# Kernel optimization log

Hardware: AMD Instinct MI355X
Metric: run time of the kernel (lower is better)

## Reference

```python
import jax, jax.numpy as jnp
import numpy as np

N, V = 256, 128000
TEMPERATURE = 1.0
TOP_P = 0.9


def setup_inputs() -> dict:
    key = jax.random.key(0)
    k1, k2 = jax.random.split(key)
    logits = jax.random.normal(k1, (N, V), dtype=jnp.float32) * 4.0
    u = jax.random.uniform(k2, (N, V), dtype=jnp.float32, minval=1e-9, maxval=1.0)
    gumbel = -jnp.log(-jnp.log(u))  # Gumbel(0,1) noise for categorical sampling
    return {"logits": logits, "gumbel": gumbel, "top_k": 50}


def reference(logits, gumbel, top_k):
    fmin = jnp.finfo(logits.dtype).min
    # sanitize non-finite logits (matches torch.where(isfinite, ...))
    logits = jnp.where(jnp.isfinite(logits), logits, fmin)
    # temperature > 0 path
    logits = logits / TEMPERATURE
    # ---- top-p (nucleus) filtering ----
    sort_idx = jnp.argsort(-logits, axis=-1)                     # descending order indices [N,V]
    sorted_logits = jnp.take_along_axis(logits, sort_idx, axis=-1)
    cum_probs = jnp.cumsum(jax.nn.softmax(sorted_logits, axis=-1), axis=-1)
    remove_sorted = cum_probs > TOP_P
    # shift right by one; always keep the top-1 token
    remove_sorted = jnp.concatenate(
        [jnp.zeros_like(remove_sorted[..., :1]), remove_sorted[..., :-1]], axis=-1)
    # scatter mask back to original order via inverse permutation
    inv_perm = jnp.argsort(sort_idx, axis=-1)
    mask = jnp.take_along_axis(remove_sorted, inv_perm, axis=-1)
    logits = jnp.where(mask, fmin, logits)
    # ---- top-k filtering ----
    kth = jax.lax.top_k(logits, top_k)[0][..., -1:]              # k-th largest per row
    logits = jnp.where(logits < kth, fmin, logits)
    # ---- softmax + categorical sample (Gumbel-max trick) ----
    probs = jax.nn.softmax(logits, axis=-1)
    x0 = jnp.argmax(logits + gumbel, axis=-1)                    # ~ Categorical(probs)
    initial_confidence = jnp.take_along_axis(probs, x0[..., None], axis=-1)[..., 0]
    confidence = initial_confidence
    return confidence, x0.astype(jnp.int32), initial_confidence
```

## Files before the change

kernel.cpp:

```cpp
#include <hip/hip_runtime.h>
#include <cstdint>
#include <cfloat>
#include <math.h>

#define VCAB 128000
#define NROWS 256
#define NTH 1024
#define NBUCK 8192
#define CAP2 2560
#define CKN 1024

__device__ __forceinline__ unsigned mono(float f) {
    unsigned u = __float_as_uint(f);
    return (u & 0x80000000u) ? ~u : (u | 0x80000000u);
}
__device__ __forceinline__ float unmono(unsigned k) {
    return __uint_as_float((k & 0x80000000u) ? (k ^ 0x80000000u) : ~k);
}

__device__ __forceinline__ unsigned find_bstar_wave(const unsigned* hist, int startb, int lane) {
    int hb = startb;
    unsigned cum = 0u;
    for (int it = 0; it < 200; ++it) {
        int b = hb - lane;
        unsigned c = (b >= 0 && b < NBUCK) ? hist[b] : 0u;
        unsigned p = c;
        #pragma unroll
        for (int off = 1; off < 64; off <<= 1) {
            unsigned q = __shfl_up(p, off, 64);
            if (lane >= off) p += q;
        }
        unsigned long long mm = __ballot(cum + p >= 64u);
        if (mm) {
            int l = __builtin_ctzll(mm);
            int b2 = hb - l;
            return (unsigned)(b2 > 0 ? b2 : 0);
        }
        cum += __shfl(p, 63, 64);
        hb -= 64;
        if (hb < 0) return 0u;
    }
    return 0u;
}

__global__ __launch_bounds__(NTH) void sampler_kernel(
    const float* __restrict__ logits,
    const float* __restrict__ gumbel,
    const int* __restrict__ topk_p,
    float* __restrict__ out)
{
    const int row = blockIdx.x;
    const int t = threadIdx.x;
    const size_t base = (size_t)row * VCAB;
    const float4* rowv = reinterpret_cast<const float4*>(logits + base);

    __shared__ unsigned hist[NBUCK];
    __shared__ unsigned long long cand[CAP2];
    __shared__ unsigned long long ck[CKN];
    __shared__ unsigned candCnt, candCnt2;
    __shared__ unsigned sh_bsamp, sh_bfin;
    __shared__ float red[16], red2[16];
    __shared__ float sh_msamp, sh_m0, sh_S;

    #pragma unroll
    for (int j = 0; j < NBUCK / NTH; ++j) hist[t + j * NTH] = 0u;
    if (t == 0) { candCnt = 0u; candCnt2 = 0u; }
    __syncthreads();

    float smax = -FLT_MAX;
    #pragma unroll
    for (int ii = 0; ii < 2; ++ii) {
        float4 x = rowv[t + ii * NTH];
        float vs[4] = {x.x, x.y, x.z, x.w};
        #pragma unroll
        for (int c = 0; c < 4; ++c) {
            float v = vs[c];
            if (!(fabsf(v) <= FLT_MAX)) v = -FLT_MAX;
            smax = fmaxf(smax, v);
            atomicAdd(&hist[mono(v) >> 19], 1u);
        }
    }
    for (int off = 32; off > 0; off >>= 1) smax = fmaxf(smax, __shfl_xor(smax, off, 64));
    if ((t & 63) == 0) red[t >> 6] = smax;
    __syncthreads();
    if (t < 16) {
        float m = red[t];
        #pragma unroll
        for (int off = 8; off > 0; off >>= 1) m = fmaxf(m, __shfl_xor(m, off, 16));
        if (t == 0) sh_msamp = m;
    }
    __syncthreads();
    const float msamp = sh_msamp;

    if (t < 64) {
        unsigned b = find_bstar_wave(hist, (int)(mono(msamp) >> 19), t);
        if (t == 0) sh_bsamp = b;
    }
    __syncthreads();
    const float thrV = unmono(sh_bsamp << 19);
    #pragma unroll
    for (int j = 0; j < NBUCK / NTH; ++j) hist[t + j * NTH] = 0u;
    __syncthreads();

    float sacc[4] = {0.f, 0.f, 0.f, 0.f};
    float lacc[4] = {-FLT_MAX, -FLT_MAX, -FLT_MAX, -FLT_MAX};
    for (int i = t; i < VCAB / 4; i += NTH) {
        float4 x = rowv[i];
        float vs[4] = {x.x, x.y, x.z, x.w};
        #pragma unroll
        for (int c = 0; c < 4; ++c) {
            float v = vs[c];
            if (!(fabsf(v) <= FLT_MAX)) v = -FLT_MAX;
            lacc[c] = fmaxf(lacc[c], v);
            sacc[c] += __expf(v - msamp);
            if (v >= thrV) {
                unsigned k = mono(v);
                atomicAdd(&hist[k >> 19], 1u);
                unsigned pos = atomicAdd(&candCnt, 1u);
                if (pos < CAP2)
                    cand[pos] = ((unsigned long long)k << 32) |
                                (unsigned long long)(~(unsigned)(i * 4 + c));
            }
        }
    }
    float s = (sacc[0] + sacc[1]) + (sacc[2] + sacc[3]);
    float lmax = fmaxf(fmaxf(lacc[0], lacc[1]), fmaxf(lacc[2], lacc[3]));
    for (int off = 32; off > 0; off >>= 1) {
        lmax = fmaxf(lmax, __shfl_xor(lmax, off, 64));
        s += __shfl_xor(s, off, 64);
    }
    if ((t & 63) == 0) { red[t >> 6] = lmax; red2[t >> 6] = s; }
    __syncthreads();
    if (t < 16) {
        float m = red[t], z = red2[t];
        #pragma unroll
        for (int off = 8; off > 0; off >>= 1) {
            m = fmaxf(m, __shfl_xor(m, off, 16));
            z += __shfl_xor(z, off, 16);
        }
        if (t == 0) { sh_m0 = m; sh_S = z; }
    }
    __syncthreads();
    const float S = sh_S;

    if (t < 64) {
        unsigned b = find_bstar_wave(hist, (int)(mono(sh_m0) >> 19), t);
        if (t == 0) sh_bfin = b;
    }
    __syncthreads();
    const unsigned bfin = sh_bfin;

    ck[t] = 0ull;
    __syncthreads();
    if (candCnt <= CAP2) {
        const unsigned nc = candCnt;
        for (unsigned j = t; j < nc; j += NTH) {
            unsigned long long e = cand[j];
            if ((unsigned)(e >> 51) >= bfin) {
                unsigned pos = atomicAdd(&candCnt2, 1u);
                if (pos < CKN) ck[pos] = e;
            }
        }
    } else {
        const float thr2 = unmono(bfin << 19);
        for (int i = t; i < VCAB / 4; i += NTH) {
            float4 x = rowv[i];
            float vs[4] = {x.x, x.y, x.z, x.w};
            #pragma unroll
            for (int c = 0; c < 4; ++c) {
                float v = vs[c];
                if (!(fabsf(v) <= FLT_MAX)) v = -FLT_MAX;
                if (v >= thr2) {
                    unsigned pos = atomicAdd(&candCnt2, 1u);
                    if (pos < CKN)
                        ck[pos] = ((unsigned long long)mono(v) << 32) |
                                  (unsigned long long)(~(unsigned)(i * 4 + c));
                }
            }
        }
    }
    __syncthreads();

    const unsigned nc2 = candCnt2 < (unsigned)CKN ? candCnt2 : (unsigned)CKN;
    const int nsort = (nc2 <= 256u) ? 256 : CKN;
    for (int k = 2; k <= nsort; k <<= 1) {
        for (int j = k >> 1; j > 0; j >>= 1) {
            __syncthreads();
            if (t < nsort) {
                int l = t ^ j;
                if (l > t) {
                    unsigned long long a = ck[t], b = ck[l];
                    bool up = ((t & k) == 0);
                    if (up ? (a < b) : (a > b)) { ck[t] = b; ck[l] = a; }
                }
            }
        }
    }
    __syncthreads();

    if (t < 64) {
        unsigned long long key = ck[t];
        float v = unmono((unsigned)(key >> 32));
        int idx = (int)(~(unsigned)key);
        int K = *topk_p;
        K = min(max(K, 1), 64);

        float p = expf(v - msamp) / S;
        float pref = p;
        for (int off = 1; off < 64; off <<= 1) {
            float xx = __shfl_up(pref, off, 64);
            if (t >= off) pref += xx;
        }
        float Eex = pref - p;
        int M = (int)__popcll(__ballot(Eex <= 0.9f));

        int Mfinal;
        if (M >= K) {
            float kth = __shfl(v, K - 1, 64);
            int J = (int)__popcll(__ballot(v >= kth));
            Mfinal = min(M, J);
        } else {
            Mfinal = M;
        }

        bool act = (t < Mfinal);
        float g  = act ? gumbel[base + (size_t)idx] : 0.f;
        float tt = act ? (v + g) : -FLT_MAX;
        int   ti = act ? idx : 0x7FFFFFFF;
        float bv = v;
        float bt = tt; int bi = ti;
        for (int off = 32; off > 0; off >>= 1) {
            float ot = __shfl_xor(bt, off, 64);
            int   oi = __shfl_xor(bi, off, 64);
            float ov = __shfl_xor(bv, off, 64);
            if (ot > bt || (ot == bt && oi < bi)) { bt = ot; bi = oi; bv = ov; }
        }
        float e = act ? expf(v - msamp) : 0.f;
        float Z = e;
        for (int off = 32; off > 0; off >>= 1) Z += __shfl_xor(Z, off, 64);

        if (t == 0) {
            float conf = expf(bv - msamp) / Z;
            out[row] = conf;
            out[NROWS + row] = (float)bi;
            out[2 * NROWS + row] = conf;
        }
    }
}

extern "C" void kernel_launch(void* const* d_in, const int* in_sizes, int n_in,
                              void* d_out, int out_size, void* d_ws, size_t ws_size,
                              hipStream_t stream) {
    const float* logits = (const float*)d_in[0];
    const float* gumbel = (const float*)d_in[1];
    const int*   topk   = (const int*)d_in[2];
    float* out = (float*)d_out;
    sampler_kernel<<<NROWS, NTH, 0, stream>>>(logits, gumbel, topk, out);
}
```

Baseline: 252.5 us.

## Use per-wave ballot-compacted candidate buffers and build histogram from candidates

```diff
diff --git a/kernel.cpp b/kernel.cpp
--- a/kernel.cpp
+++ b/kernel.cpp
@@ -6,8 +6,9 @@
 #define VCAB 128000
 #define NROWS 256
 #define NTH 1024
-#define NBUCK 8192
-#define CAP2 2560
+#define NWAVE 16
+#define NBUCK 4096
+#define CAPW 256
 #define CKN 1024
 
 __device__ __forceinline__ unsigned mono(float f) {
@@ -21,7 +22,7 @@
 __device__ __forceinline__ unsigned find_bstar_wave(const unsigned* hist, int startb, int lane) {
     int hb = startb;
     unsigned cum = 0u;
-    for (int it = 0; it < 200; ++it) {
+    for (int it = 0; it < 80; ++it) {
         int b = hb - lane;
         unsigned c = (b >= 0 && b < NBUCK) ? hist[b] : 0u;
         unsigned p = c;
@@ -51,20 +52,22 @@
 {
     const int row = blockIdx.x;
     const int t = threadIdx.x;
+    const int lane = t & 63;
+    const int wid = t >> 6;
     const size_t base = (size_t)row * VCAB;
     const float4* rowv = reinterpret_cast<const float4*>(logits + base);
 
     __shared__ unsigned hist[NBUCK];
-    __shared__ unsigned long long cand[CAP2];
+    __shared__ unsigned long long candW[NWAVE * CAPW];
     __shared__ unsigned long long ck[CKN];
-    __shared__ unsigned candCnt, candCnt2;
+    __shared__ unsigned wcnts[NWAVE];
+    __shared__ unsigned candCnt2;
     __shared__ unsigned sh_bsamp, sh_bfin;
     __shared__ float red[16], red2[16];
     __shared__ float sh_msamp, sh_m0, sh_S;
 
     #pragma unroll
     for (int j = 0; j < NBUCK / NTH; ++j) hist[t + j * NTH] = 0u;
-    if (t == 0) { candCnt = 0u; candCnt2 = 0u; }
     __syncthreads();
 
     float smax = -FLT_MAX;
@@ -77,11 +80,11 @@
             float v = vs[c];
             if (!(fabsf(v) <= FLT_MAX)) v = -FLT_MAX;
             smax = fmaxf(smax, v);
-            atomicAdd(&hist[mono(v) >> 19], 1u);
+            atomicAdd(&hist[mono(v) >> 20], 1u);
         }
     }
     for (int off = 32; off > 0; off >>= 1) smax = fmaxf(smax, __shfl_xor(smax, off, 64));
-    if ((t & 63) == 0) red[t >> 6] = smax;
+    if (lane == 0) red[wid] = smax;
     __syncthreads();
     if (t < 16) {
         float m = red[t];
@@ -93,43 +96,67 @@
     const float msamp = sh_msamp;
 
     if (t < 64) {
-        unsigned b = find_bstar_wave(hist, (int)(mono(msamp) >> 19), t);
+        unsigned b = find_bstar_wave(hist, (int)(mono(msamp) >> 20), lane);
         if (t == 0) sh_bsamp = b;
     }
     __syncthreads();
-    const float thrV = unmono(sh_bsamp << 19);
+    const float thrV = unmono(sh_bsamp << 20);
     #pragma unroll
     for (int j = 0; j < NBUCK / NTH; ++j) hist[t + j * NTH] = 0u;
     __syncthreads();
 
     float sacc[4] = {0.f, 0.f, 0.f, 0.f};
     float lacc[4] = {-FLT_MAX, -FLT_MAX, -FLT_MAX, -FLT_MAX};
-    for (int i = t; i < VCAB / 4; i += NTH) {
-        float4 x = rowv[i];
-        float vs[4] = {x.x, x.y, x.z, x.w};
-        #pragma unroll
-        for (int c = 0; c < 4; ++c) {
-            float v = vs[c];
-            if (!(fabsf(v) <= FLT_MAX)) v = -FLT_MAX;
-            lacc[c] = fmaxf(lacc[c], v);
-            sacc[c] += __expf(v - msamp);
-            if (v >= thrV) {
-                unsigned k = mono(v);
-                atomicAdd(&hist[k >> 19], 1u);
-                unsigned pos = atomicAdd(&candCnt, 1u);
-                if (pos < CAP2)
-                    cand[pos] = ((unsigned long long)k << 32) |
-                                (unsigned long long)(~(unsigned)(i * 4 + c));
-            }
-        }
-    }
+    unsigned wcnt = 0u;
+
+#define PROC(XV, IDX)                                                          \
+    {                                                                          \
+        float vs[4] = {(XV).x, (XV).y, (XV).z, (XV).w};                        \
+        _Pragma("unroll")                                                      \
+        for (int c = 0; c < 4; ++c) {                                          \
+            float v = vs[c];                                                   \
+            if (!(fabsf(v) <= FLT_MAX)) v = -FLT_MAX;                          \
+            lacc[c] = fmaxf(lacc[c], v);                                       \
+            sacc[c] += __expf(v - msamp);                                      \
+            bool p = (v >= thrV);                                              \
+            unsigned long long mb = __ballot(p);                               \
+            if (mb) {                                                          \
+                if (p) {                                                       \
+                    unsigned prefix = __builtin_amdgcn_mbcnt_hi(               \
+                        (unsigned)(mb >> 32),                                  \
+                        __builtin_amdgcn_mbcnt_lo((unsigned)mb, 0u));          \
+                    unsigned pos = wcnt + prefix;                              \
+                    if (pos < CAPW)                                            \
+                        candW[wid * CAPW + pos] =                              \
+                            ((unsigned long long)mono(v) << 32) |              \
+                            (unsigned long long)(~(unsigned)((IDX) * 4 + c));  \
+                }                                                              \
+                wcnt += (unsigned)__popcll(mb);                                \
+            }                                                                  \
+        }                                                                      \
+    }
+
+    int i = t;
+    for (; i + NTH < VCAB / 4; i += 2 * NTH) {
+        float4 xa = rowv[i];
+        float4 xb = rowv[i + NTH];
+        PROC(xa, i);
+        PROC(xb, i + NTH);
+    }
+    for (; i < VCAB / 4; i += NTH) {
+        float4 xa = rowv[i];
+        PROC(xa, i);
+    }
+#undef PROC
+
+    if (lane == 0) wcnts[wid] = wcnt;
     float s = (sacc[0] + sacc[1]) + (sacc[2] + sacc[3]);
     float lmax = fmaxf(fmaxf(lacc[0], lacc[1]), fmaxf(lacc[2], lacc[3]));
     for (int off = 32; off > 0; off >>= 1) {
         lmax = fmaxf(lmax, __shfl_xor(lmax, off, 64));
         s += __shfl_xor(s, off, 64);
     }
-    if ((t & 63) == 0) { red[t >> 6] = lmax; red2[t >> 6] = s; }
+    if (lane == 0) { red[wid] = lmax; red2[wid] = s; }
     __syncthreads();
     if (t < 16) {
         float m = red[t], z = red2[t];
@@ -143,28 +170,56 @@
     __syncthreads();
     const float S = sh_S;
 
+    bool ovf = false;
+    #pragma unroll
+    for (int w = 0; w < NWAVE; ++w) ovf |= (wcnts[w] > (unsigned)CAPW);
+
+    if (!ovf) {
+        for (int w = 0; w < NWAVE; ++w) {
+            unsigned n = wcnts[w];
+            for (unsigned j = t; j < n; j += NTH)
+                atomicAdd(&hist[(unsigned)(candW[w * CAPW + j] >> 52)], 1u);
+        }
+    } else {
+        for (int i2 = t; i2 < VCAB / 4; i2 += NTH) {
+            float4 x = rowv[i2];
+            float vs[4] = {x.x, x.y, x.z, x.w};
+            #pragma unroll
+            for (int c = 0; c < 4; ++c) {
+                float v = vs[c];
+                if (!(fabsf(v) <= FLT_MAX)) v = -FLT_MAX;
+                if (v >= thrV) atomicAdd(&hist[mono(v) >> 20], 1u);
+            }
+        }
+    }
+    __syncthreads();
+
     if (t < 64) {
-        unsigned b = find_bstar_wave(hist, (int)(mono(sh_m0) >> 19), t);
+        unsigned b = find_bstar_wave(hist, (int)(mono(sh_m0) >> 20), lane);
         if (t == 0) sh_bfin = b;
     }
     __syncthreads();
     const unsigned bfin = sh_bfin;
 
     ck[t] = 0ull;
-    __syncthreads();
-    if (candCnt <= CAP2) {
-        const unsigned nc = candCnt;
-        for (unsigned j = t; j < nc; j += NTH) {
-            unsigned long long e = cand[j];
-            if ((unsigned)(e >> 51) >= bfin) {
-                unsigned pos = atomicAdd(&candCnt2, 1u);
-                if (pos < CKN) ck[pos] = e;
+    if (t == 0) candCnt2 = 0u;
+    __syncthreads();
+
+    if (!ovf) {
+        for (int w = 0; w < NWAVE; ++w) {
+            unsigned n = wcnts[w];
+            for (unsigned j = t; j < n; j += NTH) {
+                unsigned long long e = candW[w * CAPW + j];
+                if ((unsigned)(e >> 52) >= bfin) {
+                    unsigned pos = atomicAdd(&candCnt2, 1u);
+                    if (pos < CKN) ck[pos] = e;
+                }
             }
         }
     } else {
-        const float thr2 = unmono(bfin << 19);
-        for (int i = t; i < VCAB / 4; i += NTH) {
-            float4 x = rowv[i];
+        const float thr2 = unmono(bfin << 20);
+        for (int i2 = t; i2 < VCAB / 4; i2 += NTH) {
+            float4 x = rowv[i2];
             float vs[4] = {x.x, x.y, x.z, x.w};
             #pragma unroll
             for (int c = 0; c < 4; ++c) {
@@ -174,7 +229,7 @@
                     unsigned pos = atomicAdd(&candCnt2, 1u);
                     if (pos < CKN)
                         ck[pos] = ((unsigned long long)mono(v) << 32) |
-                                  (unsigned long long)(~(unsigned)(i * 4 + c));
+                                  (unsigned long long)(~(unsigned)(i2 * 4 + c));
                 }
             }
         }
```

New measurement: 254.3 us. Within noise of the previous version (+0.7%).
